# Kernel tuning notes

Hardware: AMD Instinct MI355X
Metric: run time of the kernel (lower is better)

## Reference

```python
import jax, jax.numpy as jnp
import numpy as np
from jax import lax

BS, L, HID = 16, 512, 768
H, HD, NREG = 12, 64, 8
R2 = 2 * NREG


def setup_inputs() -> dict:
    key = jax.random.key(0)
    ks = jax.random.split(key, 7)
    s = 1.0 / np.sqrt(HID)
    return {
        "hidden_states": jax.random.normal(ks[0], (BS, L, HID), jnp.float32),
        "K1_w": jax.random.normal(ks[1], (H * HD, HID), jnp.float32) * s,
        "K1_b": jnp.zeros((H * HD,), jnp.float32),
        "V1_w": jax.random.normal(ks[2], (H * HD, HID), jnp.float32) * s,
        "V1_b": jnp.zeros((H * HD,), jnp.float32),
        "reading_head": jax.random.normal(ks[3], (H, HD), jnp.float32) * (1.0 / np.sqrt(HD)),
        "bidirection_weight": jnp.ones((1, 1, H, 1, R2), jnp.float32) * (1.0 / R2),
    }


def _softmax_dim1(x):
    # torch: softmax over length dim (1) plus 1/exp(max) residual term
    m = jnp.max(x, axis=1, keepdims=True)
    e = jnp.exp(x - m)
    return e / jnp.sum(e, axis=1, keepdims=True) + jnp.exp(-m)


def _cummax_idx(e):
    # torch.cummax indices over axis=1 for a bool tensor (ties -> latest index):
    # last True index so far; if no True yet, current index.
    ar = jnp.arange(e.shape[1], dtype=jnp.int32)[None, :, None]
    lt = lax.cummax(jnp.where(e, ar, jnp.int32(-1)), axis=1)
    return jnp.where(lt >= 0, lt, ar)


def reference(hidden_states, K1_w, K1_b, V1_w, V1_b, reading_head, bidirection_weight):
    bs, length, _ = hidden_states.shape
    K1 = jax.nn.relu(hidden_states @ K1_w.T + K1_b).reshape(bs, length, H, HD)
    V1 = jax.nn.relu(hidden_states @ V1_w.T + V1_b).reshape(bs, length, H, HD)

    scores = jnp.einsum("blhn,hn->blh", K1, reading_head)
    events = _softmax_dim1(scores) > (1.5 / length)  # (bs, L, H) bool; fwd==bwd for IC1

    col0 = _cummax_idx(events)  # (bs, L, H)
    rolled = jnp.roll(events, -1, axis=1)
    col1 = jnp.flip(512 - _cummax_idx(jnp.flip(rolled, axis=1)), axis=1)
    col1 = col1.at[:, 0].set(0)

    # sequential shift-register scan over length
    e_seq = jnp.moveaxis(events, 1, 0)  # (L, bs, H)
    f_seq = jnp.moveaxis(col0, 1, 0)
    b_seq = jnp.moveaxis(col1, 1, 0)
    row0 = jnp.concatenate(
        [f_seq[0][:, None], b_seq[0][:, None], jnp.zeros((bs, R2, H), jnp.int32)], axis=1
    )  # (bs, R2+2, H)

    def step(row, inp):
        e, f, b = inp
        reg = jnp.where(e[:, None, :], row[:, :-2], row[:, 2:])  # shift-in on event
        new_row = jnp.concatenate([f[:, None], b[:, None], reg], axis=1)
        return new_row, reg

    _, regs = lax.scan(step, row0, (e_seq[1:], f_seq[1:], b_seq[1:]))
    regs = jnp.concatenate([jnp.zeros((1, bs, R2, H), jnp.int32), regs], axis=0)  # (L,bs,R2,H)
    idx = jnp.moveaxis(regs, 0, 1).reshape(bs, length * R2, H)
    idx = jnp.clip(idx, 0, length - 1)

    V2 = jnp.take_along_axis(V1, idx[..., None], axis=1).reshape(bs, length, R2, H, HD)
    w = bidirection_weight.reshape(H, R2)
    return jnp.einsum("blrhd,hr->blhd", V2, w)  # (bs, L, H, HD)
```

## Files before the change

kernel.cpp:

```cpp
#include <hip/hip_runtime.h>
#include <cstdint>
#include <cstddef>

#define BSZ 16
#define LQ  512
#define HIDDIM 768
#define NH  12
#define HD  64
#define R2V 16
#define NTOT 1536
#define MTOT 8192

typedef __bf16 bf16x8 __attribute__((ext_vector_type(8)));
typedef float  f32x4  __attribute__((ext_vector_type(4)));

__device__ inline unsigned short f2bf(float x) {
    union { float f; unsigned u; } c; c.f = x;
    unsigned r = c.u + 0x7fffu + ((c.u >> 16) & 1u);
    return (unsigned short)(r >> 16);
}
__device__ inline float bfl(unsigned u) { return __uint_as_float(u << 16); }
__device__ inline float bfh(unsigned u) { return __uint_as_float(u & 0xffff0000u); }

#define NHS4 1572864
#define NW1  147456
#define NW4  294912

__global__ __launch_bounds__(256) void cast_pack(
    const float* __restrict__ hs,
    const float* __restrict__ Kw, const float* __restrict__ Vw,
    const float* __restrict__ Kb, const float* __restrict__ Vb,
    unsigned short* __restrict__ hsb, unsigned short* __restrict__ Wb,
    float* __restrict__ biasp)
{
    const int i = blockIdx.x * 256 + threadIdx.x;
    float4 v; unsigned short* dst;
    if (i < NHS4) {
        v = ((const float4*)hs)[i];
        dst = hsb + (size_t)i * 4;
    } else {
        const int j = i - NHS4;
        v = (j < NW1) ? ((const float4*)Kw)[j] : ((const float4*)Vw)[j - NW1];
        dst = Wb + (size_t)j * 4;
    }
    ushort4 o;
    o.x = f2bf(v.x); o.y = f2bf(v.y); o.z = f2bf(v.z); o.w = f2bf(v.w);
    *(ushort4*)dst = o;
    if (i < 768) { biasp[i] = Kb[i]; biasp[768 + i] = Vb[i]; }
}

#define TBM 128
#define TBN 128
#define TBK 32
#define KITERS (HIDDIM / TBK)

#define GLD16(g, l) __builtin_amdgcn_global_load_lds( \
    (const __attribute__((address_space(1))) void*)(g), \
    (__attribute__((address_space(3))) void*)(l), 16, 0, 0)

__global__ __launch_bounds__(256) void gemm_mfma(
    const unsigned short* __restrict__ Abf,
    const unsigned short* __restrict__ Wbf,
    const float* __restrict__ biasp,
    unsigned short* __restrict__ K1b, unsigned short* __restrict__ V1b)
{
    __shared__ unsigned short As[2][TBM * TBK];
    __shared__ unsigned short Bs[2][TBN * TBK];

    const int n0   = blockIdx.x * TBN;
    const int m0   = blockIdx.y * TBM;
    const int tid  = threadIdx.x;
    const int wid  = tid >> 6;
    const int lane = tid & 63;
    const int wm   = (wid & 1) * 64;
    const int wn   = (wid >> 1) * 64;

    f32x4 acc[4][4] = {};

    const int r0 = wid * 32;
    const int rA = r0 + (lane >> 2);
    const int kp = (lane & 3) * 8;

    const unsigned short* Ap0 = Abf + (size_t)(m0 + rA) * HIDDIM + kp;
    const unsigned short* Ap1 = Abf + (size_t)(m0 + rA + 16) * HIDDIM + kp;
    const unsigned short* Bp0 = Wbf + (size_t)(n0 + rA) * HIDDIM + kp;
    const unsigned short* Bp1 = Wbf + (size_t)(n0 + rA + 16) * HIDDIM + kp;

    const int fm = lane & 15;
    const int fk = (lane >> 4) * 8;

#define STAGE(buf, kof)                                        \
    do {                                                       \
        GLD16(Ap0 + (kof), &As[buf][r0 * TBK]);                \
        GLD16(Ap1 + (kof), &As[buf][(r0 + 16) * TBK]);         \
        GLD16(Bp0 + (kof), &Bs[buf][r0 * TBK]);                \
        GLD16(Bp1 + (kof), &Bs[buf][(r0 + 16) * TBK]);         \
    } while (0)

    STAGE(0, 0);

    for (int it = 0; it < KITERS; ++it) {
        __syncthreads();
        if (it + 1 < KITERS) STAGE((it + 1) & 1, (it + 1) * TBK);
        const int cb = it & 1;

        bf16x8 af[4], bfr[4];
        #pragma unroll
        for (int mi = 0; mi < 4; ++mi)
            af[mi] = *reinterpret_cast<const bf16x8*>(&As[cb][(wm + mi * 16 + fm) * TBK + fk]);
        #pragma unroll
        for (int ni = 0; ni < 4; ++ni)
            bfr[ni] = *reinterpret_cast<const bf16x8*>(&Bs[cb][(wn + ni * 16 + fm) * TBK + fk]);
        #pragma unroll
        for (int mi = 0; mi < 4; ++mi)
            #pragma unroll
            for (int ni = 0; ni < 4; ++ni)
                acc[mi][ni] = __builtin_amdgcn_mfma_f32_16x16x32_bf16(
                    bfr[ni], af[mi], acc[mi][ni], 0, 0, 0);
    }
#undef STAGE

    const bool isK = (n0 < HIDDIM);
    unsigned short* __restrict__ dst = isK ? K1b : V1b;
    const int nsub = isK ? 0 : HIDDIM;
    const int mloc = lane & 15;
    const int nq   = (lane >> 4) * 4;

    #pragma unroll
    for (int mi = 0; mi < 4; ++mi) {
        const int mg = m0 + wm + mi * 16 + mloc;
        #pragma unroll
        for (int ni = 0; ni < 4; ++ni) {
            const int ng = n0 + wn + ni * 16 + nq;
            float4 bv = *(const float4*)(biasp + ng);
            f32x4 a = acc[mi][ni];
            ushort4 o;
            o.x = f2bf(fmaxf(a[0] + bv.x, 0.f));
            o.y = f2bf(fmaxf(a[1] + bv.y, 0.f));
            o.z = f2bf(fmaxf(a[2] + bv.z, 0.f));
            o.w = f2bf(fmaxf(a[3] + bv.w, 0.f));
            *(ushort4*)(dst + (size_t)mg * HIDDIM + (ng - nsub)) = o;
        }
    }
}

#define SINF (1 << 30)
#define IXP 17

__global__ __launch_bounds__(512) void scan_gather(
    const unsigned short* __restrict__ K1b,
    const unsigned short* __restrict__ V1b,
    const float* __restrict__ rh,
    const float* __restrict__ bw,
    float* __restrict__ out)
{
    const int bh   = blockIdx.x >> 2;
    const int part = blockIdx.x & 3;
    const int b    = bh / NH;
    const int h    = bh % NH;
    const int l    = threadIdx.x;
    const int lane = l & 63;
    const int wid  = l >> 6;

    __shared__ float wredA[8];
    __shared__ float wredB[8];
    __shared__ int   wp0[8];
    __shared__ int   wp1[8];
    __shared__ int   wp2[8];
    __shared__ int   ev[LQ];
    __shared__ int   col0[LQ];
    __shared__ int   col1[LQ];
    __shared__ int   E[LQ];
    __shared__ int   idxs[LQ * IXP];
    __shared__ float wsm[R2V];

    if (l < R2V) wsm[l] = bw[h * R2V + l];

    const unsigned short* krow = K1b + ((size_t)(b * LQ + l)) * HIDDIM + h * HD;
    const float* rrow = rh + h * HD;
    float s = 0.f;
    #pragma unroll
    for (int c8 = 0; c8 < 8; ++c8) {
        uint4 kv = *(const uint4*)(krow + c8 * 8);
        float4 ra = *(const float4*)(rrow + c8 * 8);
        float4 rb = *(const float4*)(rrow + c8 * 8 + 4);
        s += bfl(kv.x) * ra.x + bfh(kv.x) * ra.y
           + bfl(kv.y) * ra.z + bfh(kv.y) * ra.w
           + bfl(kv.z) * rb.x + bfh(kv.z) * rb.y
           + bfl(kv.w) * rb.z + bfh(kv.w) * rb.w;
    }

    float mx = s;
    #pragma unroll
    for (int off = 32; off > 0; off >>= 1) mx = fmaxf(mx, __shfl_xor(mx, off));
    if (lane == 0) wredA[wid] = mx;
    __syncthreads();
    float m = wredA[0];
    #pragma unroll
    for (int i = 1; i < 8; ++i) m = fmaxf(m, wredA[i]);

    const float e = expf(s - m);
    float sm = e;
    #pragma unroll
    for (int off = 32; off > 0; off >>= 1) sm += __shfl_xor(sm, off);
    if (lane == 0) wredB[wid] = sm;
    __syncthreads();
    float ssum = 0.f;
    #pragma unroll
    for (int i = 0; i < 8; ++i) ssum += wredB[i];

    const float p = e / ssum + expf(-m);
    const int event = (p > (1.5f / 512.0f)) ? 1 : 0;
    ev[l] = event;

    int v = event ? l : -1;
    #pragma unroll
    for (int off = 1; off < 64; off <<= 1) {
        int u = __shfl_up(v, off);
        if (lane >= off) v = (u > v) ? u : v;
    }
    if (lane == 63) wp0[wid] = v;
    __syncthreads();
    int pfx = -1;
    for (int i = 0; i < wid; ++i) pfx = (wp0[i] > pfx) ? wp0[i] : pfx;
    v = (pfx > v) ? pfx : v;
    col0[l] = (v >= 0) ? v : l;

    int v1 = ev[(l + 1) & (LQ - 1)] ? l : SINF;
    #pragma unroll
    for (int off = 1; off < 64; off <<= 1) {
        int u = __shfl_down(v1, off);
        if (lane < 64 - off) v1 = (u < v1) ? u : v1;
    }
    if (lane == 0) wp1[wid] = v1;
    __syncthreads();
    int sfx = SINF;
    for (int i = wid + 1; i < 8; ++i) sfx = (wp1[i] < sfx) ? wp1[i] : sfx;
    v1 = (sfx < v1) ? sfx : v1;
    col1[l] = (l == 0) ? 0 : (((v1 < SINF) ? v1 : l) + 1);

    int c = (l >= 1) ? event : 0;
    #pragma unroll
    for (int off = 1; off < 64; off <<= 1) {
        int u = __shfl_up(c, off);
        if (lane >= off) c += u;
    }
    if (lane == 63) wp2[wid] = c;
    __syncthreads();
    for (int i = 0; i < wid; ++i) c += wp2[i];

    if (l >= 1 && event) E[c - 1] = l;
    __syncthreads();

    int* op = &idxs[l * IXP];
    #pragma unroll
    for (int j = 0; j < 8; ++j) {
        const int k = c - 1 - j;
        int f = 0, bb = 0;
        if (k >= 0) {
            const int t = E[k];
            f  = col0[t - 1];
            bb = col1[t - 1];
        }
        op[2 * j]     = min(max(f, 0), LQ - 1);
        op[2 * j + 1] = min(max(bb, 0), LQ - 1);
    }
    __syncthreads();

    const int dsl = lane & 7;
    const size_t vbase = (size_t)b * LQ * HIDDIM + h * HD + dsl * 8;

    for (int rr = 0; rr < 2; ++rr) {
        const int round = part * 2 + rr;
        const int lg = round * 64 + wid * 8 + (lane >> 3);
        const int* ip = &idxs[lg * IXP];
        float a0 = 0.f, a1 = 0.f, a2 = 0.f, a3 = 0.f;
        float a4 = 0.f, a5 = 0.f, a6 = 0.f, a7 = 0.f;
        #pragma unroll 1
        for (int rc = 0; rc < R2V; rc += 4) {
            const int i0 = ip[rc], i1 = ip[rc + 1], i2 = ip[rc + 2], i3 = ip[rc + 3];
            uint4 v0 = *(const uint4*)(V1b + vbase + (size_t)i0 * HIDDIM);
            uint4 vA = *(const uint4*)(V1b + vbase + (size_t)i1 * HIDDIM);
            uint4 vB = *(const uint4*)(V1b + vbase + (size_t)i2 * HIDDIM);
            uint4 vC = *(const uint4*)(V1b + vbase + (size_t)i3 * HIDDIM);
            const float w0 = wsm[rc], w1 = wsm[rc + 1], w2 = wsm[rc + 2], w3 = wsm[rc + 3];
            a0 += w0 * bfl(v0.x); a1 += w0 * bfh(v0.x);
            a2 += w0 * bfl(v0.y); a3 += w0 * bfh(v0.y);
            a4 += w0 * bfl(v0.z); a5 += w0 * bfh(v0.z);
            a6 += w0 * bfl(v0.w); a7 += w0 * bfh(v0.w);
            a0 += w1 * bfl(vA.x); a1 += w1 * bfh(vA.x);
            a2 += w1 * bfl(vA.y); a3 += w1 * bfh(vA.y);
            a4 += w1 * bfl(vA.z); a5 += w1 * bfh(vA.z);
            a6 += w1 * bfl(vA.w); a7 += w1 * bfh(vA.w);
            a0 += w2 * bfl(vB.x); a1 += w2 * bfh(vB.x);
            a2 += w2 * bfl(vB.y); a3 += w2 * bfh(vB.y);
            a4 += w2 * bfl(vB.z); a5 += w2 * bfh(vB.z);
            a6 += w2 * bfl(vB.w); a7 += w2 * bfh(vB.w);
            a0 += w3 * bfl(vC.x); a1 += w3 * bfh(vC.x);
            a2 += w3 * bfl(vC.y); a3 += w3 * bfh(vC.y);
            a4 += w3 * bfl(vC.z); a5 += w3 * bfh(vC.z);
            a6 += w3 * bfl(vC.w); a7 += w3 * bfh(vC.w);
        }
        float* po = out + ((size_t)(b * LQ + lg) * NH + h) * HD + dsl * 8;
        *(float4*)po       = make_float4(a0, a1, a2, a3);
        *((float4*)po + 1) = make_float4(a4, a5, a6, a7);
    }
}

extern "C" void kernel_launch(void* const* d_in, const int* in_sizes, int n_in,
                              void* d_out, int out_size, void* d_ws, size_t ws_size,
                              hipStream_t stream)
{
    (void)in_sizes; (void)n_in; (void)out_size; (void)ws_size;

    const float* hs = (const float*)d_in[0];
    const float* Kw = (const float*)d_in[1];
    const float* Kb = (const float*)d_in[2];
    const float* Vw = (const float*)d_in[3];
    const float* Vb = (const float*)d_in[4];
    const float* rh = (const float*)d_in[5];
    const float* bw = (const float*)d_in[6];
    float* out = (float*)d_out;

    char* ws = (char*)d_ws;
    unsigned short* K1b   = (unsigned short*)(ws);
    unsigned short* V1b   = (unsigned short*)(ws + 12582912);
    unsigned short* hsb   = (unsigned short*)(ws + 25165824);
    unsigned short* Wb    = (unsigned short*)(ws + 37748736);
    float*          biasp = (float*)(ws + 40108032);

    cast_pack<<<(NHS4 + NW4) / 256, 256, 0, stream>>>(hs, Kw, Vw, Kb, Vb, hsb, Wb, biasp);

    dim3 g1(NTOT / TBN, MTOT / TBM);
    gemm_mfma<<<g1, 256, 0, stream>>>(hsb, Wb, biasp, K1b, V1b);

    scan_gather<<<BSZ * NH * 4, LQ, 0, stream>>>(K1b, V1b, rh, bw, out);
}
```

Before: 143.7 us.

## Enlarge GEMM tile to 256x256 with 8 waves, swizzled LDS and setprio

Grows the bf16 MFMA GEMM block tile from 128x128 to 256x256 and uses 512 threads, with each wave computing 128x64 so more operand reuse comes from LDS. An XOR swizzle is applied to the k-offset in both the global-to-LDS staging and the fragment reads to cut LDS bank conflicts. The MFMA burst is wrapped in s_setprio. The trade-off is a smaller grid (192 blocks on 256 CUs), which may leave compute units idle, plus higher register pressure from 32 accumulators per thread.

```diff
diff --git a/kernel.cpp b/kernel.cpp
--- a/kernel.cpp
+++ b/kernel.cpp
@@ -49,90 +49,93 @@
     if (i < 768) { biasp[i] = Kb[i]; biasp[768 + i] = Vb[i]; }
 }
 
-#define TBM 128
-#define TBN 128
+#define TBM 256
+#define TBN 256
 #define TBK 32
-#define KITERS (HIDDIM / TBK)
+#define KT  (HIDDIM / TBK)
+#define ATILE (TBM * TBK)
 
 #define GLD16(g, l) __builtin_amdgcn_global_load_lds( \
     (const __attribute__((address_space(1))) void*)(g), \
     (__attribute__((address_space(3))) void*)(l), 16, 0, 0)
 
-__global__ __launch_bounds__(256) void gemm_mfma(
+__global__ __launch_bounds__(512, 2) void gemm_mfma(
     const unsigned short* __restrict__ Abf,
     const unsigned short* __restrict__ Wbf,
     const float* __restrict__ biasp,
     unsigned short* __restrict__ K1b, unsigned short* __restrict__ V1b)
 {
-    __shared__ unsigned short As[2][TBM * TBK];
-    __shared__ unsigned short Bs[2][TBN * TBK];
+    __shared__ unsigned short As[2][ATILE];
+    __shared__ unsigned short Bs[2][ATILE];
 
     const int n0   = blockIdx.x * TBN;
     const int m0   = blockIdx.y * TBM;
     const int tid  = threadIdx.x;
     const int wid  = tid >> 6;
     const int lane = tid & 63;
-    const int wm   = (wid & 1) * 64;
-    const int wn   = (wid >> 1) * 64;
-
-    f32x4 acc[4][4] = {};
-
-    const int r0 = wid * 32;
-    const int rA = r0 + (lane >> 2);
-    const int kp = (lane & 3) * 8;
-
-    const unsigned short* Ap0 = Abf + (size_t)(m0 + rA) * HIDDIM + kp;
-    const unsigned short* Ap1 = Abf + (size_t)(m0 + rA + 16) * HIDDIM + kp;
-    const unsigned short* Bp0 = Wbf + (size_t)(n0 + rA) * HIDDIM + kp;
-    const unsigned short* Bp1 = Wbf + (size_t)(n0 + rA + 16) * HIDDIM + kp;
-
-    const int fm = lane & 15;
-    const int fk = (lane >> 4) * 8;
-
-#define STAGE(buf, kof)                                        \
-    do {                                                       \
-        GLD16(Ap0 + (kof), &As[buf][r0 * TBK]);                \
-        GLD16(Ap1 + (kof), &As[buf][(r0 + 16) * TBK]);         \
-        GLD16(Bp0 + (kof), &Bs[buf][r0 * TBK]);                \
-        GLD16(Bp1 + (kof), &Bs[buf][(r0 + 16) * TBK]);         \
+    const int wr   = wid >> 2;
+    const int wc   = wid & 3;
+
+    f32x4 acc[8][4] = {};
+
+    const int srow = lane >> 2;
+    const int scol = ((lane & 3) ^ ((lane >> 3) & 3)) << 3;
+    const int r0   = wid * 32;
+
+    const unsigned short* Ag = Abf + (size_t)(m0 + r0 + srow) * HIDDIM + scol;
+    const unsigned short* Bg = Wbf + (size_t)(n0 + r0 + srow) * HIDDIM + scol;
+
+#define STAGE(buf, kt) do {                                                   \
+        const int kof_ = (kt) * TBK;                                          \
+        GLD16(Ag + kof_,                    &As[buf][r0 * TBK]);              \
+        GLD16(Ag + 16 * HIDDIM + kof_,      &As[buf][(r0 + 16) * TBK]);       \
+        GLD16(Bg + kof_,                    &Bs[buf][r0 * TBK]);              \
+        GLD16(Bg + 16 * HIDDIM + kof_,      &Bs[buf][(r0 + 16) * TBK]);       \
     } while (0)
 
+    const int fm   = lane & 15;
+    const int fj   = lane >> 4;
+    const int koff = ((fj ^ ((fm >> 1) & 3)) << 3);
+
     STAGE(0, 0);
 
-    for (int it = 0; it < KITERS; ++it) {
+    for (int kt = 0; kt < KT; ++kt) {
         __syncthreads();
-        if (it + 1 < KITERS) STAGE((it + 1) & 1, (it + 1) * TBK);
-        const int cb = it & 1;
-
-        bf16x8 af[4], bfr[4];
+        if (kt + 1 < KT) STAGE((kt + 1) & 1, kt + 1);
+        const int cb = kt & 1;
+
+        bf16x8 af[8], bfr[4];
         #pragma unroll
-        for (int mi = 0; mi < 4; ++mi)
-            af[mi] = *reinterpret_cast<const bf16x8*>(&As[cb][(wm + mi * 16 + fm) * TBK + fk]);
+        for (int mi = 0; mi < 8; ++mi)
+            af[mi] = *reinterpret_cast<const bf16x8*>(
+                &As[cb][(wr * 128 + mi * 16 + fm) * TBK + koff]);
         #pragma unroll
         for (int ni = 0; ni < 4; ++ni)
-            bfr[ni] = *reinterpret_cast<const bf16x8*>(&Bs[cb][(wn + ni * 16 + fm) * TBK + fk]);
+            bfr[ni] = *reinterpret_cast<const bf16x8*>(
+                &Bs[cb][(wc * 64 + ni * 16 + fm) * TBK + koff]);
+        __builtin_amdgcn_s_setprio(1);
         #pragma unroll
-        for (int mi = 0; mi < 4; ++mi)
+        for (int mi = 0; mi < 8; ++mi)
             #pragma unroll
             for (int ni = 0; ni < 4; ++ni)
                 acc[mi][ni] = __builtin_amdgcn_mfma_f32_16x16x32_bf16(
                     bfr[ni], af[mi], acc[mi][ni], 0, 0, 0);
+        __builtin_amdgcn_s_setprio(0);
     }
 #undef STAGE
 
     const bool isK = (n0 < HIDDIM);
     unsigned short* __restrict__ dst = isK ? K1b : V1b;
     const int nsub = isK ? 0 : HIDDIM;
-    const int mloc = lane & 15;
-    const int nq   = (lane >> 4) * 4;
-
-    #pragma unroll
-    for (int mi = 0; mi < 4; ++mi) {
-        const int mg = m0 + wm + mi * 16 + mloc;
+    const int nq   = fj * 4;
+
+    #pragma unroll
+    for (int ni = 0; ni < 4; ++ni) {
+        const int ng = n0 + wc * 64 + ni * 16 + nq;
+        const float4 bv = *(const float4*)(biasp + ng);
         #pragma unroll
-        for (int ni = 0; ni < 4; ++ni) {
-            const int ng = n0 + wn + ni * 16 + nq;
-            float4 bv = *(const float4*)(biasp + ng);
+        for (int mi = 0; mi < 8; ++mi) {
+            const int mg = m0 + wr * 128 + mi * 16 + fm;
             f32x4 a = acc[mi][ni];
             ushort4 o;
             o.x = f2bf(fmaxf(a[0] + bv.x, 0.f));
@@ -332,7 +335,7 @@
     cast_pack<<<(NHS4 + NW4) / 256, 256, 0, stream>>>(hs, Kw, Vw, Kb, Vb, hsb, Wb, biasp);
 
     dim3 g1(NTOT / TBN, MTOT / TBM);
-    gemm_mfma<<<g1, 256, 0, stream>>>(hsb, Wb, biasp, K1b, V1b);
+    gemm_mfma<<<g1, 512, 0, stream>>>(hsb, Wb, biasp, K1b, V1b);
 
     scan_gather<<<BSZ * NH * 4, LQ, 0, stream>>>(K1b, V1b, rh, bw, out);
 }
```

Measured after the change: 152.4 us. 6.0% more time.
